# Kernel optimization log

Measured on AMD Instinct MI355X. Metric: run time of the kernel, lower is better.

## Reference

```python
import jax, jax.numpy as jnp
import numpy as np

HID, HEADS = 512, 8
C_DIM, H_DIM, W_DIM = 512, 64, 64
THETA = 100000000.0


def _angles(c, h, w, theta):
    # matches precompute_freqs_cis: angles whose polar form is freqs_cis
    n_f = c // 4
    freqs = 1.0 / theta ** (jnp.arange(0, c, 4)[:n_f].astype(jnp.float32) / c)  # (c//4,)
    th = jnp.arange(h, dtype=jnp.float32)
    tw = jnp.arange(w, dtype=jnp.float32)
    T = jnp.stack([jnp.broadcast_to(th[:, None], (h, w)),
                   jnp.broadcast_to(tw[None, :], (h, w))], axis=2)  # (h, w, 2)
    # torch cat [T*f0, T*f1, ...] along dim 2 == (h, w, c//4, 2) reshaped
    return (T[:, :, None, :] * freqs[None, None, :, None]).reshape(h, w, c // 2)


def setup_inputs() -> dict:
    key = jax.random.key(0)
    ks = jax.random.split(key, 9)
    B, S = 2, H_DIM * W_DIM
    s = 0.02
    return {
        "query": jax.random.normal(ks[0], (B, S, HID), jnp.float32),
        "key": jax.random.normal(ks[1], (B, S, HID), jnp.float32),
        "value": jax.random.normal(ks[2], (B, S, HID), jnp.float32),
        "Wq": jax.random.normal(ks[3], (HID, HID), jnp.float32) * s,
        "bq": jax.random.normal(ks[4], (HID,), jnp.float32) * s,
        "Wk": jax.random.normal(ks[5], (HID, HID), jnp.float32) * s,
        "bk": jax.random.normal(ks[6], (HID,), jnp.float32) * s,
        "Wv": jax.random.normal(ks[7], (HID, HID), jnp.float32) * s,
        "bv": jax.random.normal(ks[8], (HID,), jnp.float32) * s,
        "h": H_DIM,
        "w": W_DIM,
        "c": HID,
    }


def reference(query, key, value, Wq, bq, Wk, bk, Wv, bv, h, w, c):
    B = query.shape[0]
    hd = HID // HEADS
    ang = _angles(C_DIM, H_DIM, W_DIM, THETA)[:h, :w].reshape(h * w, c // 2)
    cos, sin = jnp.cos(ang), jnp.sin(ang)  # (S, c//2)

    Q = query @ Wq.T + bq
    K = key @ Wk.T + bk
    V = value @ Wv.T + bv

    def rot(x):  # complex multiply on consecutive pairs, in real arithmetic
        x2 = x.reshape(B, -1, c // 2, 2)
        xr, xi = x2[..., 0], x2[..., 1]
        return jnp.stack([xr * cos - xi * sin, xr * sin + xi * cos], axis=-1).reshape(B, -1, c)

    Q, K = rot(Q), rot(K)

    def heads(x):
        return x.reshape(B, -1, HEADS, hd).transpose(0, 2, 1, 3)  # (B, H, S, hd)

    Qh, Kh, Vh = heads(Q), heads(K), heads(V)
    # NOTE: original divides by head_dim (self.scale), not sqrt(head_dim)
    att = jnp.einsum('bhqd,bhkd->bhqk', Qh, Kh) / hd
    att = jax.nn.softmax(att, axis=-1)
    out = jnp.einsum('bhqk,bhkd->bhqd', att, Vh)
    return out.transpose(0, 2, 1, 3).reshape(B, -1, HID)
```

## Files before the change

kernel.cpp:

```cpp
#include <hip/hip_runtime.h>
#include <hip/hip_bf16.h>

#define S_LEN 4096
#define HDIM  64
#define NH    8

#define XFRAG_OFF 0
#define WFRAG_OFF 12582912
#define QKV_OFF   13369344
#define WS_NEED_BYTES ((size_t)(13369344 + 12582912) * 2)

typedef short s16x8 __attribute__((ext_vector_type(8)));
typedef float f32x16 __attribute__((ext_vector_type(16)));
typedef unsigned short u16x4 __attribute__((ext_vector_type(4)));
typedef int i32x2 __attribute__((ext_vector_type(2)));

union FragU {
    s16x8 v;
    unsigned int u[4];
    unsigned short h[8];
};

static __device__ __forceinline__ unsigned int pack2_bf16(float a, float b) {
    __hip_bfloat162 h2 = __float22bfloat162_rn(float2{a, b});
    union { __hip_bfloat162 h; unsigned int u; } cv;
    cv.h = h2;
    return cv.u;
}

static __device__ __forceinline__ unsigned short to_bf16(float a) {
    __hip_bfloat16 h = __float2bfloat16(a);
    union { __hip_bfloat16 h; unsigned short u; } cv;
    cv.h = h;
    return cv.u;
}

#define Q_PRESCALE 0.022542110f
#define FREQ_L2 0.20762050593046f

__global__ __launch_bounds__(256) void conv_frag3(
    const float* __restrict__ qx, const float* __restrict__ kx,
    const float* __restrict__ vx,
    const float* __restrict__ Wq, const float* __restrict__ Wk,
    const float* __restrict__ Wv,
    unsigned short* __restrict__ xdst, unsigned short* __restrict__ wdst)
{
    __shared__ __align__(16) unsigned short slds[16640];

    const int z  = blockIdx.z;
    const int bx = blockIdx.x;
    const int tid  = threadIdx.x;
    const int w    = tid >> 6;
    const int lane = tid & 63;

    const float* src;
    unsigned short* dst;
    if (bx < 256) {
        src = ((z == 0) ? qx : ((z == 1) ? kx : vx)) + (size_t)bx * 32 * 512;
        dst = xdst + (size_t)z * 4194304 + (size_t)bx * 16384;
    } else {
        const int s = bx - 256;
        src = ((z == 0) ? Wq : ((z == 1) ? Wk : Wv)) + (size_t)s * 32 * 512;
        dst = wdst + (size_t)z * 262144 + (size_t)s * 16384;
    }

    #pragma unroll
    for (int i = 0; i < 8; ++i) {
        const int r = w * 8 + i;
        const float4* p = (const float4*)(src + (size_t)r * 512 + lane * 8);
        float4 x0 = p[0], x1 = p[1];
        FragU f;
        f.u[0] = pack2_bf16(x0.x, x0.y);
        f.u[1] = pack2_bf16(x0.z, x0.w);
        f.u[2] = pack2_bf16(x1.x, x1.y);
        f.u[3] = pack2_bf16(x1.z, x1.w);
        *(s16x8*)(slds + (lane >> 1) * 520 + ((lane & 1) * 32 + r) * 8) = f.v;
    }
    __syncthreads();

    #pragma unroll
    for (int i = 0; i < 8; ++i) {
        const int kc = w * 8 + i;
        s16x8 v = *(const s16x8*)(slds + kc * 520 + lane * 8);
        *(s16x8*)(dst + kc * 512 + lane * 8) = v;
    }
}

static __device__ __forceinline__ void qkv_epilogue(
    int z, const f32x16 acc[2][2], int m0, int n0, int c31, int hi,
    const float* __restrict__ bias, unsigned short* __restrict__ dst_base)
{
    if (z < 2) {
        unsigned short* dst = dst_base + (size_t)z * 4194304;
        #pragma unroll
        for (int nt = 0; nt < 2; ++nt) {
            const int s_g = n0 + nt * 32 + c31;
            const int b   = s_g >> 12;
            const int s   = s_g & 4095;
            const float pos0 = (float)(s >> 6);
            const float pos1 = (float)(s & 63);
            #pragma unroll
            for (int mt = 0; mt < 2; ++mt) {
                #pragma unroll
                for (int g = 0; g < 4; ++g) {
                    const int o_b = m0 + mt * 32 + 8 * g + 4 * hi;
                    const float4 bb = *(const float4*)(bias + o_b);
                    float v0 = acc[mt][nt][4 * g + 0] + bb.x;
                    float v1 = acc[mt][nt][4 * g + 1] + bb.y;
                    float v2 = acc[mt][nt][4 * g + 2] + bb.z;
                    float v3 = acc[mt][nt][4 * g + 3] + bb.w;
                    const float fr0 = exp2f(-(float)(o_b >> 2) * FREQ_L2);
                    float sn0, cs0, sn1, cs1;
                    __sincosf(pos0 * fr0, &sn0, &cs0);
                    __sincosf(pos1 * fr0, &sn1, &cs1);
                    float r0 = v0 * cs0 - v1 * sn0;
                    float r1 = v0 * sn0 + v1 * cs0;
                    float r2 = v2 * cs1 - v3 * sn1;
                    float r3 = v2 * sn1 + v3 * cs1;
                    if (z == 0) { r0 *= Q_PRESCALE; r1 *= Q_PRESCALE; r2 *= Q_PRESCALE; r3 *= Q_PRESCALE; }
                    const int bh = b * NH + (o_b >> 6);
                    const int k6 = o_b & 63;
                    u16x4 pk;
                    pk.x = to_bf16(r0); pk.y = to_bf16(r1);
                    pk.z = to_bf16(r2); pk.w = to_bf16(r3);
                    const size_t off = (size_t)bh * 262144 + (s >> 5) * 2048
                                     + (k6 >> 4) * 512 + (((k6 >> 3) & 1) * 32 + (s & 31)) * 8 + (k6 & 7);
                    *(u16x4*)(dst + off) = pk;
                }
            }
        }
    } else {
        unsigned short* dst = dst_base + 8388608;
        #pragma unroll
        for (int nt = 0; nt < 2; ++nt) {
            const int o  = n0 + nt * 32 + c31;
            const float bv_ = bias[o];
            const int d = o & 63, hh = o >> 6;
            #pragma unroll
            for (int mt = 0; mt < 2; ++mt) {
                #pragma unroll
                for (int g = 0; g < 4; ++g) {
                    const int s_b = m0 + mt * 32 + 8 * g + 4 * hi;
                    const int b = s_b >> 12;
                    const int s = s_b & 4095;
                    const int bh = b * NH + hh;
                    u16x4 pk;
                    pk.x = to_bf16(acc[mt][nt][4 * g + 0] + bv_);
                    pk.y = to_bf16(acc[mt][nt][4 * g + 1] + bv_);
                    pk.z = to_bf16(acc[mt][nt][4 * g + 2] + bv_);
                    pk.w = to_bf16(acc[mt][nt][4 * g + 3] + bv_);
                    const size_t off = (size_t)bh * 262144 + (s >> 5) * 2048 + (d >> 5) * 1024
                                     + ((s >> 4) & 1) * 512 + (((s >> 3) & 1) * 32 + (d & 31)) * 8 + (s & 7);
                    *(u16x4*)(dst + off) = pk;
                }
            }
        }
    }
}

__global__ __launch_bounds__(256) void qkv_gemm_rope(
    const unsigned short* __restrict__ xf, const unsigned short* __restrict__ wf,
    const float* __restrict__ bq, const float* __restrict__ bk,
    const float* __restrict__ bv, unsigned short* __restrict__ dst_base)
{
    const int z = blockIdx.z;
    const float* bias = (z == 0) ? bq : ((z == 1) ? bk : bv);
    const unsigned short* X = xf + (size_t)z * 4194304;
    const unsigned short* W = wf + (size_t)z * 262144;

    const int tid  = threadIdx.x;
    const int wv   = tid >> 6;
    const int lane = tid & 63;
    const int c31  = lane & 31;
    const int hi   = lane >> 5;
    const int wm   = wv >> 1, wn = wv & 1;

    int m0, n0;
    const unsigned short *A, *B;
    if (z < 2) {
        m0 = blockIdx.y * 128 + wm * 64;
        n0 = blockIdx.x * 128 + wn * 64;
        A = W; B = X;
    } else {
        m0 = blockIdx.x * 128 + wm * 64;
        n0 = blockIdx.y * 128 + wn * 64;
        A = X; B = W;
    }

    const unsigned short* ap0 = A + (size_t)(m0 >> 5) * 16384 + lane * 8;
    const unsigned short* ap1 = ap0 + 16384;
    const unsigned short* bp0 = B + (size_t)(n0 >> 5) * 16384 + lane * 8;
    const unsigned short* bp1 = bp0 + 16384;

    f32x16 acc[2][2];
    #pragma unroll
    for (int a = 0; a < 2; ++a)
    #pragma unroll
    for (int b = 0; b < 2; ++b)
    #pragma unroll
    for (int r = 0; r < 16; ++r) acc[a][b][r] = 0.f;

    #pragma unroll 4
    for (int kc = 0; kc < 32; ++kc) {
        const int ko = kc * 512;
        s16x8 a0 = *(const s16x8*)(ap0 + ko);
        s16x8 a1 = *(const s16x8*)(ap1 + ko);
        s16x8 b0 = *(const s16x8*)(bp0 + ko);
        s16x8 b1 = *(const s16x8*)(bp1 + ko);
        acc[0][0] = __builtin_amdgcn_mfma_f32_32x32x16_bf16(a0, b0, acc[0][0], 0, 0, 0);
        acc[0][1] = __builtin_amdgcn_mfma_f32_32x32x16_bf16(a0, b1, acc[0][1], 0, 0, 0);
        acc[1][0] = __builtin_amdgcn_mfma_f32_32x32x16_bf16(a1, b0, acc[1][0], 0, 0, 0);
        acc[1][1] = __builtin_amdgcn_mfma_f32_32x32x16_bf16(a1, b1, acc[1][1], 0, 0, 0);
    }

    qkv_epilogue(z, acc, m0, n0, c31, hi, bias, dst_base);
}

__global__ __launch_bounds__(256) void qkv_rope_f32(
    const float* __restrict__ q_in, const float* __restrict__ k_in,
    const float* __restrict__ v_in,
    const float* __restrict__ Wq, const float* __restrict__ bq,
    const float* __restrict__ Wk, const float* __restrict__ bk,
    const float* __restrict__ Wv, const float* __restrict__ bv,
    unsigned short* __restrict__ dst_base)
{
    const int z = blockIdx.z;
    const float* Xr = (z == 0) ? q_in : ((z == 1) ? k_in : v_in);
    const float* Wr = (z == 0) ? Wq   : ((z == 1) ? Wk   : Wv);
    const float* bias = (z == 0) ? bq : ((z == 1) ? bk : bv);

    const int tid  = threadIdx.x;
    const int wv   = tid >> 6;
    const int lane = tid & 63;
    const int c31  = lane & 31;
    const int hi   = lane >> 5;
    const int wm   = wv >> 1, wn = wv & 1;

    int m0, n0;
    const float *A, *B;
    if (z < 2) { m0 = blockIdx.y * 128 + wm * 64; n0 = blockIdx.x * 128 + wn * 64; A = Wr; B = Xr; }
    else       { m0 = blockIdx.x * 128 + wm * 64; n0 = blockIdx.y * 128 + wn * 64; A = Xr; B = Wr; }

    f32x16 acc[2][2];
    #pragma unroll
    for (int a = 0; a < 2; ++a)
    #pragma unroll
    for (int b = 0; b < 2; ++b)
    #pragma unroll
    for (int r = 0; r < 16; ++r) acc[a][b][r] = 0.f;

    for (int kc = 0; kc < 32; ++kc) {
        const int kofs = kc * 16 + hi * 8;
        FragU a_f[2], b_f[2];
        #pragma unroll
        for (int mt = 0; mt < 2; ++mt) {
            const float4* p = (const float4*)(A + (size_t)(m0 + mt * 32 + c31) * 512 + kofs);
            float4 x0 = p[0], x1 = p[1];
            a_f[mt].u[0] = pack2_bf16(x0.x, x0.y);
            a_f[mt].u[1] = pack2_bf16(x0.z, x0.w);
            a_f[mt].u[2] = pack2_bf16(x1.x, x1.y);
            a_f[mt].u[3] = pack2_bf16(x1.z, x1.w);
        }
        #pragma unroll
        for (int nt = 0; nt < 2; ++nt) {
            const float4* p = (const float4*)(B + (size_t)(n0 + nt * 32 + c31) * 512 + kofs);
            float4 x0 = p[0], x1 = p[1];
            b_f[nt].u[0] = pack2_bf16(x0.x, x0.y);
            b_f[nt].u[1] = pack2_bf16(x0.z, x0.w);
            b_f[nt].u[2] = pack2_bf16(x1.x, x1.y);
            b_f[nt].u[3] = pack2_bf16(x1.z, x1.w);
        }
        #pragma unroll
        for (int mt = 0; mt < 2; ++mt)
        #pragma unroll
        for (int nt = 0; nt < 2; ++nt)
            acc[mt][nt] = __builtin_amdgcn_mfma_f32_32x32x16_bf16(
                a_f[mt].v, b_f[nt].v, acc[mt][nt], 0, 0, 0);
    }

    qkv_epilogue(z, acc, m0, n0, c31, hi, bias, dst_base);
}

static __device__ __forceinline__ s16x8 build_pfrag(
    unsigned int a0, unsigned int a1, unsigned int a2, unsigned int a3)
{
    i32x2 r02 = __builtin_amdgcn_permlane32_swap((int)a0, (int)a2, false, false);
    i32x2 r13 = __builtin_amdgcn_permlane32_swap((int)a1, (int)a3, false, false);
    FragU pb;
    pb.u[0] = (unsigned int)r02.x;
    pb.u[1] = (unsigned int)r13.x;
    pb.u[2] = (unsigned int)r02.y;
    pb.u[3] = (unsigned int)r13.y;
    return pb.v;
}

__global__ __launch_bounds__(256, 2) void flash_attn_st(
    const unsigned short* __restrict__ qkv, float* __restrict__ out)
{
    __shared__ __align__(16) unsigned char smem[32768 + 1024];
    unsigned short* sQ = (unsigned short*)smem;
    float* sOb = (float*)smem;
    float* sL  = (float*)(smem + 32768);

    const int tid  = threadIdx.x;
    const int wv   = tid >> 6;
    const int lane = tid & 63;
    const int c31  = lane & 31;
    const int hi   = lane >> 5;
    const int id   = blockIdx.x;
    const int bh   = id & 15;
    const int q0   = (id >> 4) * 64;

    const unsigned short* Qb  = qkv + (size_t)bh * 262144;
    const unsigned short* Kb  = qkv + (size_t)4194304 + (size_t)bh * 262144;
    const unsigned short* Vtb = qkv + (size_t)8388608 + (size_t)bh * 262144;

    #pragma unroll
    for (int i = 0; i < 2; ++i) {
        const int idx   = tid + i * 256;
        const int chunk = idx >> 6;
        const int ln    = idx & 63;
        *(s16x8*)(sQ + chunk * 512 + ln * 8) =
            *(const s16x8*)(Qb + (size_t)((q0 >> 5) + (chunk >> 2)) * 2048 + (chunk & 3) * 512 + ln * 8);
    }
    __syncthreads();

    s16x8 qf0[4], qf1[4];
    #pragma unroll
    for (int kc = 0; kc < 4; ++kc) {
        qf0[kc] = *(const s16x8*)(sQ + kc * 512 + lane * 8);
        qf1[kc] = *(const s16x8*)(sQ + 2048 + kc * 512 + lane * 8);
    }

    f32x16 o_acc[2][2];
    #pragma unroll
    for (int a = 0; a < 2; ++a)
    #pragma unroll
    for (int b = 0; b < 2; ++b)
    #pragma unroll
    for (int r = 0; r < 16; ++r) o_acc[a][b][r] = 0.f;
    float l_acc[2] = {0.f, 0.f};

    const unsigned short* kp = Kb  + (size_t)wv * 2048 + lane * 8;
    const unsigned short* vp = Vtb + (size_t)wv * 2048 + lane * 8;

    s16x8 ka[4];
    #pragma unroll
    for (int kc = 0; kc < 4; ++kc)
        ka[kc] = *(const s16x8*)(kp + kc * 512);

    for (int it = 0; it < 32; ++it) {
        s16x8 va[2][2];
        va[0][0] = *(const s16x8*)(vp);
        va[0][1] = *(const s16x8*)(vp + 512);
        va[1][0] = *(const s16x8*)(vp + 1024);
        va[1][1] = *(const s16x8*)(vp + 1536);
        vp += 8192;

        f32x16 st0, st1;
        #pragma unroll
        for (int r = 0; r < 16; ++r) { st0[r] = 0.f; st1[r] = 0.f; }
        __builtin_amdgcn_s_setprio(1);
        #pragma unroll
        for (int kc = 0; kc < 4; ++kc)
            st0 = __builtin_amdgcn_mfma_f32_32x32x16_bf16(ka[kc], qf0[kc], st0, 0, 0, 0);
        #pragma unroll
        for (int kc = 0; kc < 4; ++kc)
            st1 = __builtin_amdgcn_mfma_f32_32x32x16_bf16(ka[kc], qf1[kc], st1, 0, 0, 0);
        __builtin_amdgcn_s_setprio(0);

        kp += 8192;
        if (it < 31) {
            #pragma unroll
            for (int kc = 0; kc < 4; ++kc)
                ka[kc] = *(const s16x8*)(kp + kc * 512);
        }

        unsigned int up0[8];
        {
            float ls0 = 0.f, ls1 = 0.f;
            #pragma unroll
            for (int qq = 0; qq < 8; ++qq) {
                float p0 = __builtin_amdgcn_exp2f(st0[2 * qq]);
                float p1 = __builtin_amdgcn_exp2f(st0[2 * qq + 1]);
                ls0 += p0; ls1 += p1;
                up0[qq] = pack2_bf16(p0, p1);
            }
            l_acc[0] += ls0 + ls1;
        }

        #pragma unroll
        for (int k2 = 0; k2 < 2; ++k2) {
            s16x8 pfrag = build_pfrag(up0[4 * k2 + 0], up0[4 * k2 + 1],
                                      up0[4 * k2 + 2], up0[4 * k2 + 3]);
            __builtin_amdgcn_s_setprio(1);
            #pragma unroll
            for (int dt = 0; dt < 2; ++dt)
                o_acc[dt][0] = __builtin_amdgcn_mfma_f32_32x32x16_bf16(
                    va[dt][k2], pfrag, o_acc[dt][0], 0, 0, 0);
            __builtin_amdgcn_s_setprio(0);
        }

        unsigned int up1[8];
        {
            float ls0 = 0.f, ls1 = 0.f;
            #pragma unroll
            for (int qq = 0; qq < 8; ++qq) {
                float p0 = __builtin_amdgcn_exp2f(st1[2 * qq]);
                float p1 = __builtin_amdgcn_exp2f(st1[2 * qq + 1]);
                ls0 += p0; ls1 += p1;
                up1[qq] = pack2_bf16(p0, p1);
            }
            l_acc[1] += ls0 + ls1;
        }

        #pragma unroll
        for (int k2 = 0; k2 < 2; ++k2) {
            s16x8 pfrag = build_pfrag(up1[4 * k2 + 0], up1[4 * k2 + 1],
                                      up1[4 * k2 + 2], up1[4 * k2 + 3]);
            __builtin_amdgcn_s_setprio(1);
            #pragma unroll
            for (int dt = 0; dt < 2; ++dt)
                o_acc[dt][1] = __builtin_amdgcn_mfma_f32_32x32x16_bf16(
                    va[dt][k2], pfrag, o_acc[dt][1], 0, 0, 0);
            __builtin_amdgcn_s_setprio(0);
        }
    }

    {
        float l0 = l_acc[0] + __shfl_xor(l_acc[0], 32);
        float l1 = l_acc[1] + __shfl_xor(l_acc[1], 32);
        if (lane < 32) {
            sL[(wv * 2 + 0) * 32 + lane] = l0;
            sL[(wv * 2 + 1) * 32 + lane] = l1;
        }
    }
    __syncthreads();

    if (wv == 1 || wv == 2) {
        float* buf = sOb + (wv - 1) * 4096;
        #pragma unroll
        for (int dt = 0; dt < 2; ++dt)
        #pragma unroll
        for (int qt = 0; qt < 2; ++qt)
        #pragma unroll
        for (int r = 0; r < 16; ++r) {
            const int d = dt * 32 + (r & 3) + 8 * (r >> 2) + 4 * hi;
            buf[d * 64 + qt * 32 + c31] = o_acc[dt][qt][r];
        }
    }
    __syncthreads();
    if (wv == 0 || wv == 3) {
        const float* buf = sOb + ((wv == 0) ? 0 : 4096);
        #pragma unroll
        for (int dt = 0; dt < 2; ++dt)
        #pragma unroll
        for (int qt = 0; qt < 2; ++qt)
        #pragma unroll
        for (int r = 0; r < 16; ++r) {
            const int d = dt * 32 + (r & 3) + 8 * (r >> 2) + 4 * hi;
            o_acc[dt][qt][r] += buf[d * 64 + qt * 32 + c31];
        }
    }
    __syncthreads();
    if (wv == 3) {
        #pragma unroll
        for (int dt = 0; dt < 2; ++dt)
        #pragma unroll
        for (int qt = 0; qt < 2; ++qt)
        #pragma unroll
        for (int r = 0; r < 16; ++r) {
            const int d = dt * 32 + (r & 3) + 8 * (r >> 2) + 4 * hi;
            sOb[d * 64 + qt * 32 + c31] = o_acc[dt][qt][r];
        }
    }
    __syncthreads();
    if (wv == 0) {
        #pragma unroll
        for (int dt = 0; dt < 2; ++dt)
        #pragma unroll
        for (int qt = 0; qt < 2; ++qt)
        #pragma unroll
        for (int r = 0; r < 16; ++r) {
            const int d = dt * 32 + (r & 3) + 8 * (r >> 2) + 4 * hi;
            o_acc[dt][qt][r] += sOb[d * 64 + qt * 32 + c31];
        }
        const int b  = bh >> 3;
        const int hh = bh & 7;
        #pragma unroll
        for (int qt = 0; qt < 2; ++qt) {
            const float lsum = sL[(0 * 2 + qt) * 32 + c31] + sL[(1 * 2 + qt) * 32 + c31]
                             + sL[(2 * 2 + qt) * 32 + c31] + sL[(3 * 2 + qt) * 32 + c31];
            const float rinv = 1.f / lsum;
            const int s = q0 + qt * 32 + c31;
            float* orow = out + ((size_t)b * S_LEN + s) * 512 + hh * 64;
            #pragma unroll
            for (int dt = 0; dt < 2; ++dt) {
                #pragma unroll
                for (int g = 0; g < 4; ++g) {
                    float4 vv;
                    vv.x = o_acc[dt][qt][4 * g + 0] * rinv;
                    vv.y = o_acc[dt][qt][4 * g + 1] * rinv;
                    vv.z = o_acc[dt][qt][4 * g + 2] * rinv;
                    vv.w = o_acc[dt][qt][4 * g + 3] * rinv;
                    *(float4*)(orow + dt * 32 + 8 * g + 4 * hi) = vv;
                }
            }
        }
    }
}

extern "C" void kernel_launch(void* const* d_in, const int* in_sizes, int n_in,
                              void* d_out, int out_size, void* d_ws, size_t ws_size,
                              hipStream_t stream) {
    (void)in_sizes; (void)n_in; (void)out_size;
    const float* q_in = (const float*)d_in[0];
    const float* k_in = (const float*)d_in[1];
    const float* v_in = (const float*)d_in[2];
    const float* Wq   = (const float*)d_in[3];
    const float* bq   = (const float*)d_in[4];
    const float* Wk   = (const float*)d_in[5];
    const float* bk   = (const float*)d_in[6];
    const float* Wv   = (const float*)d_in[7];
    const float* bv   = (const float*)d_in[8];
    unsigned short* ws = (unsigned short*)d_ws;
    float* out = (float*)d_out;

    if (ws_size >= WS_NEED_BYTES) {
        conv_frag3<<<dim3(272, 1, 3), 256, 0, stream>>>(
            q_in, k_in, v_in, Wq, Wk, Wv, ws + XFRAG_OFF, ws + WFRAG_OFF);
        qkv_gemm_rope<<<dim3(64, 4, 3), 256, 0, stream>>>(
            ws + XFRAG_OFF, ws + WFRAG_OFF, bq, bk, bv, ws + QKV_OFF);
        flash_attn_st<<<dim3(1024), 256, 0, stream>>>(ws + QKV_OFF, out);
    } else {
        qkv_rope_f32<<<dim3(64, 4, 3), 256, 0, stream>>>(
            q_in, k_in, v_in, Wq, bq, Wk, bk, Wv, bv, ws);
        flash_attn_st<<<dim3(1024), 256, 0, stream>>>(ws, out);
    }
}
```

Before: 212.5 us.

## Stage QKV GEMM operands through double-buffered LDS via global_load_lds

The QKV projection GEMM now copies A and B fragment tiles into a double-buffered shared-memory stage with direct global-to-LDS loads, prefetching the next k-chunk while MFMAs consume the current one. Before, each wave loaded its own fragments straight from global memory, so tiles shared across waves were fetched more than once and load latency was exposed. This adds LDS use and a barrier per stage, which may reduce occupancy.

```diff
diff --git a/kernel.cpp b/kernel.cpp
--- a/kernel.cpp
+++ b/kernel.cpp
@@ -163,6 +163,8 @@
     const float* __restrict__ bq, const float* __restrict__ bk,
     const float* __restrict__ bv, unsigned short* __restrict__ dst_base)
 {
+    __shared__ __align__(16) unsigned char gsm[2][16384];
+
     const int z = blockIdx.z;
     const float* bias = (z == 0) ? bq : ((z == 1) ? bk : bv);
     const unsigned short* X = xf + (size_t)z * 4194304;
@@ -175,22 +177,19 @@
     const int hi   = lane >> 5;
     const int wm   = wv >> 1, wn = wv & 1;
 
-    int m0, n0;
+    int m0, n0, ablk, bblk;
     const unsigned short *A, *B;
     if (z < 2) {
         m0 = blockIdx.y * 128 + wm * 64;
         n0 = blockIdx.x * 128 + wn * 64;
-        A = W; B = X;
+        A = W; B = X; ablk = blockIdx.y; bblk = blockIdx.x;
     } else {
         m0 = blockIdx.x * 128 + wm * 64;
         n0 = blockIdx.y * 128 + wn * 64;
-        A = X; B = W;
-    }
-
-    const unsigned short* ap0 = A + (size_t)(m0 >> 5) * 16384 + lane * 8;
-    const unsigned short* ap1 = ap0 + 16384;
-    const unsigned short* bp0 = B + (size_t)(n0 >> 5) * 16384 + lane * 8;
-    const unsigned short* bp1 = bp0 + 16384;
+        A = X; B = W; ablk = blockIdx.x; bblk = blockIdx.y;
+    }
+    const unsigned short* Ab = A + (size_t)ablk * 4 * 16384;
+    const unsigned short* Bb = B + (size_t)bblk * 4 * 16384;
 
     f32x16 acc[2][2];
     #pragma unroll
@@ -200,18 +199,44 @@
     #pragma unroll
     for (int r = 0; r < 16; ++r) acc[a][b][r] = 0.f;
 
-    #pragma unroll 4
-    for (int kc = 0; kc < 32; ++kc) {
-        const int ko = kc * 512;
-        s16x8 a0 = *(const s16x8*)(ap0 + ko);
-        s16x8 a1 = *(const s16x8*)(ap1 + ko);
-        s16x8 b0 = *(const s16x8*)(bp0 + ko);
-        s16x8 b1 = *(const s16x8*)(bp1 + ko);
-        acc[0][0] = __builtin_amdgcn_mfma_f32_32x32x16_bf16(a0, b0, acc[0][0], 0, 0, 0);
-        acc[0][1] = __builtin_amdgcn_mfma_f32_32x32x16_bf16(a0, b1, acc[0][1], 0, 0, 0);
-        acc[1][0] = __builtin_amdgcn_mfma_f32_32x32x16_bf16(a1, b0, acc[1][0], 0, 0, 0);
-        acc[1][1] = __builtin_amdgcn_mfma_f32_32x32x16_bf16(a1, b1, acc[1][1], 0, 0, 0);
-    }
+#define QSTAGE(BUF, KC0)                                                      \
+    do {                                                                      \
+        _Pragma("unroll")                                                     \
+        for (int j = 0; j < 4; ++j) {                                         \
+            const int c_  = wv * 4 + j;                                       \
+            const int ko_ = c_ >> 3;                                          \
+            const int tl_ = c_ & 3;                                           \
+            const unsigned short* g_ = (((c_ >> 2) & 1) ? Bb : Ab)            \
+                + (size_t)tl_ * 16384 + (size_t)((KC0) + ko_) * 512 + lane * 8; \
+            __builtin_amdgcn_global_load_lds(                                 \
+                (const __attribute__((address_space(1))) void*)g_,            \
+                (__attribute__((address_space(3))) void*)(&gsm[BUF][c_ * 1024]), \
+                16, 0, 0);                                                    \
+        }                                                                     \
+    } while (0)
+
+    QSTAGE(0, 0);
+    __syncthreads();
+
+    const int a_t0 = wm * 2, b_t0 = wn * 2;
+    for (int s = 0; s < 16; ++s) {
+        const int cur = s & 1;
+        if (s < 15) QSTAGE(cur ^ 1, (s + 1) * 2);
+        #pragma unroll
+        for (int ko = 0; ko < 2; ++ko) {
+            const unsigned char* base = gsm[cur] + ko * 8192;
+            s16x8 a0 = *(const s16x8*)(base + (size_t)(a_t0 + 0) * 1024 + lane * 16);
+            s16x8 a1 = *(const s16x8*)(base + (size_t)(a_t0 + 1) * 1024 + lane * 16);
+            s16x8 b0 = *(const s16x8*)(base + 4096 + (size_t)(b_t0 + 0) * 1024 + lane * 16);
+            s16x8 b1 = *(const s16x8*)(base + 4096 + (size_t)(b_t0 + 1) * 1024 + lane * 16);
+            acc[0][0] = __builtin_amdgcn_mfma_f32_32x32x16_bf16(a0, b0, acc[0][0], 0, 0, 0);
+            acc[0][1] = __builtin_amdgcn_mfma_f32_32x32x16_bf16(a0, b1, acc[0][1], 0, 0, 0);
+            acc[1][0] = __builtin_amdgcn_mfma_f32_32x32x16_bf16(a1, b0, acc[1][0], 0, 0, 0);
+            acc[1][1] = __builtin_amdgcn_mfma_f32_32x32x16_bf16(a1, b1, acc[1][1], 0, 0, 0);
+        }
+        __syncthreads();
+    }
+#undef QSTAGE
 
     qkv_epilogue(z, acc, m0, n0, c31, hi, bias, dst_base);
 }
```

Result: no change. 208.7 us (median of 2 runs) (-1.8%).
